# Kernel optimization log

Measured on AMD Instinct MI355X. Metric: run time of the kernel, lower is better.

## Reference

```python
import jax, jax.numpy as jnp
import numpy as np
from jax import lax

NPOINT = 1024
RADIUS = 0.2
NSAMPLE = 32


def fps(xyz, npoint):
    """Furthest point sampling on one cloud. xyz: (N,3) -> (npoint,) int32."""
    n = xyz.shape[0]
    init_d = jnp.full((n,), 1e10, xyz.dtype)

    def body(carry, _):
        dists, last_idx = carry
        last = xyz[last_idx]
        d = jnp.sum((xyz - last) ** 2, axis=-1)
        dists = jnp.minimum(dists, d)
        nxt = jnp.argmax(dists).astype(jnp.int32)
        return (dists, nxt), nxt

    (_, _), idxs = lax.scan(body, (init_d, jnp.int32(0)), None, length=npoint - 1)
    return jnp.concatenate([jnp.zeros((1,), jnp.int32), idxs])


def ball_query(xyz, new_xyz, radius, nsample):
    """First `nsample` points of xyz within `radius` of each center (pad with first hit).
    xyz: (N,3), new_xyz: (S,3) -> (S,nsample) int32."""
    n = xyz.shape[0]
    d2 = jnp.sum((new_xyz[:, None, :] - xyz[None, :, :]) ** 2, axis=-1)  # (S,N)
    cand = jnp.where(d2 < radius * radius, jnp.arange(n, dtype=jnp.int32)[None, :], n)
    idx = jnp.sort(cand, axis=1)[:, :nsample]                            # (S,K)
    first = jnp.where(idx[:, :1] == n, 0, idx[:, :1])
    return jnp.where(idx == n, first, idx)


def setup_inputs() -> dict:
    key = jax.random.key(0)
    ks = jax.random.split(key, 8)
    C_in = 64 + 3  # features + relative xyz
    W1 = jax.random.normal(ks[0], (64, C_in), jnp.float32) * (1.0 / np.sqrt(C_in))
    b1 = jnp.zeros((64,), jnp.float32)
    W2 = jax.random.normal(ks[1], (128, 64), jnp.float32) * (1.0 / np.sqrt(64))
    b2 = jnp.zeros((128,), jnp.float32)
    W3 = jax.random.normal(ks[2], (256, 128), jnp.float32) * (1.0 / np.sqrt(128))
    b3 = jnp.zeros((256,), jnp.float32)
    xyz = jax.random.uniform(ks[3], (8, 4096, 3), jnp.float32)
    features = jax.random.normal(ks[4], (8, 4096, 64), jnp.float32)
    return {"xyz": xyz, "features": features, "W1": W1, "b1": b1,
            "W2": W2, "b2": b2, "W3": W3, "b3": b3}


def reference(xyz, features, W1, b1, W2, b2, W3, b3):
    def per_batch(xyz_b, feat_b):
        fps_idx = fps(xyz_b, NPOINT)                      # (S,)
        new_xyz = xyz_b[fps_idx]                          # (S,3)
        idx = ball_query(xyz_b, new_xyz, RADIUS, NSAMPLE)  # (S,K)
        g_xyz = xyz_b[idx] - new_xyz[:, None, :]          # (S,K,3) relative coords
        g_feat = feat_b[idx]                              # (S,K,C)
        g = jnp.concatenate([g_xyz, g_feat], axis=-1)     # (S,K,3+C)
        x = jnp.transpose(g, (2, 0, 1))                   # (C',S,K)
        for W, b in ((W1, b1), (W2, b2), (W3, b3)):       # 1x1 conv + ReLU stack
            x = jax.nn.relu(jnp.einsum('oc,csk->osk', W, x) + b[:, None, None])
        return new_xyz, jnp.max(x, axis=-1), fps_idx      # max-pool over nsample

    new_xyz, new_features, sample_inds = jax.vmap(per_batch)(xyz, features)
    return new_xyz, new_features, sample_inds
```

## Files before the change

kernel.cpp:

```cpp
#include <hip/hip_runtime.h>
#include <stdint.h>

#define N_PTS 4096
#define S_PTS 1024
#define K_SAMP 32

typedef __attribute__((ext_vector_type(8))) short bf16x8;
typedef __attribute__((ext_vector_type(4))) float f32x4;

#define GT1_S 104
#define GT2_S 72
#define GT3_S 136

__device__ __forceinline__ short f2b(float f){
  unsigned u = __float_as_uint(f);
  u = u + 0x7fffu + ((u >> 16) & 1u);
  return (short)(u >> 16);
}

#define DPP_QUAD_XOR1 0xB1
#define DPP_QUAD_XOR2 0x4E
#define DPP_ROW_HMIRR 0x141
#define DPP_ROW_MIRR  0x140
#define DPP_ROW_BC15  0x142
#define DPP_ROW_BC31  0x143

template<int CTRL>
__device__ __forceinline__ unsigned long long kstep(unsigned long long k){
  unsigned lo = (unsigned)k, hi = (unsigned)(k >> 32);
  unsigned lo2 = (unsigned)__builtin_amdgcn_update_dpp((int)lo, (int)lo, CTRL, 0xF, 0xF, false);
  unsigned hi2 = (unsigned)__builtin_amdgcn_update_dpp((int)hi, (int)hi, CTRL, 0xF, 0xF, false);
  unsigned long long ok = ((unsigned long long)hi2 << 32) | lo2;
  return ok > k ? ok : k;
}

__global__ __launch_bounds__(256) void fps_kernel(const float* __restrict__ xyz,
                                                  float* __restrict__ out_newxyz,
                                                  float* __restrict__ out_inds){
  __shared__ float4 c4[N_PTS];
  __shared__ unsigned long long slots[2][4];
  const int b = blockIdx.x;
  const int t = threadIdx.x;
  const int lane = t & 63;
  const int w = t >> 6;
  const float* xb = xyz + (size_t)b * N_PTS * 3;

  float px[16], py[16], pz[16], dist[16];
#pragma unroll
  for (int j = 0; j < 16; ++j){
    int p = j * 256 + t;
    float x = xb[p*3+0], y = xb[p*3+1], z = xb[p*3+2];
    px[j] = x; py[j] = y; pz[j] = z; dist[j] = 1e10f;
    c4[p] = make_float4(x, y, z, 0.0f);
  }
  __syncthreads();

  float lx, ly, lz;
  { float4 c0 = c4[0]; lx = c0.x; ly = c0.y; lz = c0.z; }
  if (t == 0){
    out_inds[(size_t)b * S_PTS] = 0.0f;
    out_newxyz[(size_t)b*S_PTS*3 + 0] = lx;
    out_newxyz[(size_t)b*S_PTS*3 + 1] = ly;
    out_newxyz[(size_t)b*S_PTS*3 + 2] = lz;
  }

  for (int it = 1; it < S_PTS; ++it){
    float bv = -1.0f; int bj = 0;
#pragma unroll
    for (int j = 0; j < 16; ++j){
      float dx = __fsub_rn(px[j], lx);
      float dy = __fsub_rn(py[j], ly);
      float dz = __fsub_rn(pz[j], lz);
      float d  = __fadd_rn(__fadd_rn(__fmul_rn(dx,dx), __fmul_rn(dy,dy)), __fmul_rn(dz,dz));
      float nd = fminf(dist[j], d);
      dist[j] = nd;
      bool gt = nd > bv;
      bv = gt ? nd : bv;
      bj = gt ? j  : bj;
    }
    int bi = bj * 256 + t;
    unsigned long long k = ((unsigned long long)__float_as_uint(bv) << 32)
                         | (unsigned)(~bi);

    k = kstep<DPP_QUAD_XOR1>(k);
    k = kstep<DPP_QUAD_XOR2>(k);
    k = kstep<DPP_ROW_HMIRR>(k);
    k = kstep<DPP_ROW_MIRR >(k);
    k = kstep<DPP_ROW_BC15 >(k);
    k = kstep<DPP_ROW_BC31 >(k);

    if (lane == 63) slots[it & 1][w] = k;
    __syncthreads();

    unsigned long long sk = slots[it & 1][lane & 3];
    sk = kstep<DPP_QUAD_XOR1>(sk);
    sk = kstep<DPP_QUAD_XOR2>(sk);
    int cur = (int)(~(unsigned)sk);

    float4 cc = c4[cur];
    lx = cc.x; ly = cc.y; lz = cc.z;
    if (t == 0){
      out_inds[(size_t)b*S_PTS + it] = (float)cur;
      out_newxyz[((size_t)b*S_PTS + it)*3 + 0] = lx;
      out_newxyz[((size_t)b*S_PTS + it)*3 + 1] = ly;
      out_newxyz[((size_t)b*S_PTS + it)*3 + 2] = lz;
    }
  }
}

__global__ void wconv_kernel(const float* __restrict__ W1,
                             const float* __restrict__ W2,
                             const float* __restrict__ W3,
                             short* __restrict__ ws_w){
  short* w1 = ws_w;
  short* w2 = ws_w + 64*96;
  short* w3 = ws_w + 64*96 + 128*64;
  int t = blockIdx.x * blockDim.x + threadIdx.x;
  int stride = gridDim.x * blockDim.x;
  for (int i = t; i < 64*96; i += stride){
    int m = i / 96, k = i - m*96;
    float v = 0.0f;
    if (k < 64)      v = W1[m*67 + 3 + k];
    else if (k < 67) v = W1[m*67 + (k - 64)];
    w1[i] = f2b(v);
  }
  for (int i = t; i < 128*64;  i += stride) w2[i] = f2b(W2[i]);
  for (int i = t; i < 256*128; i += stride) w3[i] = f2b(W3[i]);
}

__global__ __launch_bounds__(256) void ballquery_kernel(const float* __restrict__ xyz,
                                                        const float* __restrict__ newxyz,
                                                        int* __restrict__ idx_ws){
  const int lane = threadIdx.x & 63;
  const int c = blockIdx.x * 4 + (threadIdx.x >> 6);
  const int b = c >> 10;
  const float* xb = xyz + (size_t)b * N_PTS * 3;
  const float cx = newxyz[(size_t)c*3+0];
  const float cy = newxyz[(size_t)c*3+1];
  const float cz = newxyz[(size_t)c*3+2];
  const float R2 = 0.2f * 0.2f;
  int* idxp = idx_ws + (size_t)c * K_SAMP;
  int have = 0, first = -1;
  for (int chunk = 0; chunk < 64 && have < K_SAMP; ++chunk){
    int p = chunk * 64 + lane;
    float dx = __fsub_rn(xb[p*3+0], cx);
    float dy = __fsub_rn(xb[p*3+1], cy);
    float dz = __fsub_rn(xb[p*3+2], cz);
    float d2 = __fadd_rn(__fadd_rn(__fmul_rn(dx,dx), __fmul_rn(dy,dy)), __fmul_rn(dz,dz));
    bool hit = d2 < R2;
    unsigned long long mask = __ballot(hit);
    if (mask){
      if (first < 0) first = chunk*64 + (__ffsll(mask) - 1);
      int pre = __popcll(mask & ((1ull << lane) - 1ull));
      if (hit && (have + pre) < K_SAMP) idxp[have + pre] = p;
      have += __popcll(mask);
      if (have > K_SAMP) have = K_SAMP;
    }
  }
  if (first < 0) first = 0;
  if (lane < K_SAMP - have) idxp[have + lane] = first;
}

template<int M, int KC, int KPAD, int GS_IN, int GS_OUT>
__device__ __forceinline__ void layer_mfma(const short* __restrict__ Wl,
                                           const short* gin, short* gout,
                                           const float* __restrict__ sbias_l,
                                           int w, int quad, int col){
  for (int m0 = w*16; m0 < M; m0 += 64){
    f32x4 acc0 = {0,0,0,0}, acc1 = {0,0,0,0};
#pragma unroll
    for (int kc = 0; kc < KC; ++kc){
      bf16x8 a  = *reinterpret_cast<const bf16x8*>(Wl + (size_t)(m0+col)*KPAD + kc*32 + quad*8);
      bf16x8 b0 = *reinterpret_cast<const bf16x8*>(gin + col*GS_IN + kc*32 + quad*8);
      bf16x8 b1 = *reinterpret_cast<const bf16x8*>(gin + (16+col)*GS_IN + kc*32 + quad*8);
      acc0 = __builtin_amdgcn_mfma_f32_16x16x32_bf16(a, b0, acc0, 0, 0, 0);
      acc1 = __builtin_amdgcn_mfma_f32_16x16x32_bf16(a, b1, acc1, 0, 0, 0);
    }
    int rbase = m0 + quad*4;
    unsigned long long P0 = 0ull, P1 = 0ull;
#pragma unroll
    for (int r = 0; r < 4; ++r){
      float bias = sbias_l[rbase + r];
      unsigned long long q0 = (unsigned short)f2b(fmaxf(acc0[r] + bias, 0.0f));
      unsigned long long q1 = (unsigned short)f2b(fmaxf(acc1[r] + bias, 0.0f));
      P0 |= q0 << (16*r);
      P1 |= q1 << (16*r);
    }
    *reinterpret_cast<unsigned long long*>(&gout[col*GS_OUT + rbase])      = P0;
    *reinterpret_cast<unsigned long long*>(&gout[(16+col)*GS_OUT + rbase]) = P1;
  }
}

__global__ __launch_bounds__(256) void mlp_kernel(const float* __restrict__ xyz,
                                                  const float* __restrict__ feat,
                                                  const float* __restrict__ b1,
                                                  const float* __restrict__ b2,
                                                  const float* __restrict__ b3,
                                                  const float* __restrict__ newxyz,
                                                  const int* __restrict__ idx_ws,
                                                  const short* __restrict__ ws_w,
                                                  float* __restrict__ pooled){
  __shared__ __align__(16) short gT1[32*GT1_S];
  __shared__ __align__(16) short gT2[32*GT2_S];
  __shared__ __align__(16) short gT3[32*GT3_S];
  __shared__ int   sidx[32];
  __shared__ float sbias[448];
  const int t = threadIdx.x;
  const int c = blockIdx.x;
  const int b = c >> 10;
  const int lane = t & 63;
  const int w = t >> 6;
  const int quad = lane >> 4;
  const int col = lane & 15;

  const short* w1 = ws_w;
  const short* w2 = ws_w + 64*96;
  const short* w3 = ws_w + 64*96 + 128*64;

  if (t < 32) sidx[t] = idx_ws[(size_t)c*K_SAMP + t];
  for (int i = t; i < 448; i += 256)
    sbias[i] = (i < 64) ? b1[i] : (i < 192) ? b2[i-64] : b3[i-192];
  for (int i = t; i < 32*GT1_S; i += 256) gT1[i] = 0;
  __syncthreads();

  {
    int p = t >> 3, q = t & 7;
    int src = sidx[p];
    const float* fr = feat + ((size_t)b * N_PTS + src) * 64 + q*8;
    unsigned u[4];
#pragma unroll
    for (int jj = 0; jj < 4; ++jj){
      unsigned lo = (unsigned short)f2b(fr[2*jj]);
      unsigned hi = (unsigned short)f2b(fr[2*jj+1]);
      u[jj] = lo | (hi << 16);
    }
    uint4 v; v.x = u[0]; v.y = u[1]; v.z = u[2]; v.w = u[3];
    *reinterpret_cast<uint4*>(&gT1[p*GT1_S + q*8]) = v;
  }
  if (t < 32){
    int src = sidx[t];
    const float* pr = xyz + ((size_t)b * N_PTS + src) * 3;
    float cx = newxyz[(size_t)c*3+0];
    float cy = newxyz[(size_t)c*3+1];
    float cz = newxyz[(size_t)c*3+2];
    gT1[t*GT1_S + 64] = f2b(__fsub_rn(pr[0], cx));
    gT1[t*GT1_S + 65] = f2b(__fsub_rn(pr[1], cy));
    gT1[t*GT1_S + 66] = f2b(__fsub_rn(pr[2], cz));
  }
  __syncthreads();

  layer_mfma<64, 3, 96, GT1_S, GT2_S>(w1, gT1, gT2, sbias, w, quad, col);
  __syncthreads();
  layer_mfma<128, 2, 64, GT2_S, GT3_S>(w2, gT2, gT3, sbias + 64, w, quad, col);
  __syncthreads();

  for (int m0 = w*16; m0 < 256; m0 += 64){
    f32x4 acc0 = {0,0,0,0}, acc1 = {0,0,0,0};
#pragma unroll
    for (int kc = 0; kc < 4; ++kc){
      bf16x8 a  = *reinterpret_cast<const bf16x8*>(w3 + (size_t)(m0+col)*128 + kc*32 + quad*8);
      bf16x8 b0 = *reinterpret_cast<const bf16x8*>(gT3 + col*GT3_S + kc*32 + quad*8);
      bf16x8 b1 = *reinterpret_cast<const bf16x8*>(gT3 + (16+col)*GT3_S + kc*32 + quad*8);
      acc0 = __builtin_amdgcn_mfma_f32_16x16x32_bf16(a, b0, acc0, 0, 0, 0);
      acc1 = __builtin_amdgcn_mfma_f32_16x16x32_bf16(a, b1, acc1, 0, 0, 0);
    }
    float vm[4];
#pragma unroll
    for (int r = 0; r < 4; ++r) vm[r] = fmaxf(acc0[r], acc1[r]);
#pragma unroll
    for (int off = 1; off < 16; off <<= 1){
#pragma unroll
      for (int r = 0; r < 4; ++r) vm[r] = fmaxf(vm[r], __shfl_xor(vm[r], off, 16));
    }
    if (col == 0){
#pragma unroll
      for (int r = 0; r < 4; ++r){
        int ch = m0 + quad*4 + r;
        pooled[(size_t)c*256 + ch] = fmaxf(vm[r] + sbias[192 + ch], 0.0f);
      }
    }
  }
}

__global__ __launch_bounds__(256) void transpose_kernel(const float* __restrict__ pooled,
                                                        float* __restrict__ outf){
  __shared__ float tile[64][65];
  int b  = blockIdx.z;
  int s0 = blockIdx.x * 64;
  int c0 = blockIdx.y * 64;
#pragma unroll
  for (int k = 0; k < 16; ++k){
    int idx = threadIdx.x + k*256;
    int si = idx >> 6, ci = idx & 63;
    tile[si][ci] = pooled[((size_t)b*S_PTS + s0 + si)*256 + c0 + ci];
  }
  __syncthreads();
#pragma unroll
  for (int k = 0; k < 16; ++k){
    int idx = threadIdx.x + k*256;
    int ci = idx >> 6, si = idx & 63;
    outf[((size_t)b*256 + c0 + ci)*S_PTS + s0 + si] = tile[si][ci];
  }
}

extern "C" void kernel_launch(void* const* d_in, const int* in_sizes, int n_in,
                              void* d_out, int out_size, void* d_ws, size_t ws_size,
                              hipStream_t stream){
  const float* xyz  = (const float*)d_in[0];
  const float* feat = (const float*)d_in[1];
  const float* W1   = (const float*)d_in[2];
  const float* b1   = (const float*)d_in[3];
  const float* W2   = (const float*)d_in[4];
  const float* b2   = (const float*)d_in[5];
  const float* W3   = (const float*)d_in[6];
  const float* b3   = (const float*)d_in[7];

  float* out        = (float*)d_out;
  float* out_newxyz = out;
  float* out_feat   = out + 24576;
  float* out_inds   = out + 24576 + 2097152;

  char*  ws     = (char*)d_ws;
  short* ws_w   = (short*)ws;
  int*   idx_ws = (int*)(ws + 94208);
  float* pooled = (float*)(ws + 94208 + 1048576);

  wconv_kernel<<<32, 256, 0, stream>>>(W1, W2, W3, ws_w);
  fps_kernel<<<8, 256, 0, stream>>>(xyz, out_newxyz, out_inds);
  ballquery_kernel<<<2048, 256, 0, stream>>>(xyz, out_newxyz, idx_ws);
  mlp_kernel<<<8192, 256, 0, stream>>>(xyz, feat, b1, b2, b3, out_newxyz,
                                       idx_ws, ws_w, pooled);
  transpose_kernel<<<dim3(16, 4, 8), 256, 0, stream>>>(pooled, out_feat);
}
```

Baseline: 796.8 us.

## Pack FPS distance math, tree-reduce argmax, buffer outputs in LDS

The furthest-point-sampling loop now does the distance arithmetic two points at a time with packed v_pk_add/v_pk_mul f32 instructions. The serial per-thread argmax over 16 points becomes a pairwise tree, which shortens the dependency chain. Per-iteration global stores by thread 0 are replaced by writes to an LDS ring, flushed with coalesced stores after the loop. Rounding should stay the same because packed ops are separate mul and add without FMA. Tie-breaking in the tree still favours the lower index, as the strict > did before.

```diff
diff --git a/kernel.cpp b/kernel.cpp
--- a/kernel.cpp
+++ b/kernel.cpp
@@ -7,6 +7,7 @@
 
 typedef __attribute__((ext_vector_type(8))) short bf16x8;
 typedef __attribute__((ext_vector_type(4))) float f32x4;
+typedef __attribute__((ext_vector_type(2))) float f32x2;
 
 #define GT1_S 104
 #define GT2_S 72
@@ -16,6 +17,13 @@
   unsigned u = __float_as_uint(f);
   u = u + 0x7fffu + ((u >> 16) & 1u);
   return (short)(u >> 16);
+}
+
+__device__ __forceinline__ f32x2 pk_add(f32x2 a, f32x2 b){
+  f32x2 d; asm("v_pk_add_f32 %0, %1, %2" : "=v"(d) : "v"(a), "v"(b)); return d;
+}
+__device__ __forceinline__ f32x2 pk_mul(f32x2 a, f32x2 b){
+  f32x2 d; asm("v_pk_mul_f32 %0, %1, %2" : "=v"(d) : "v"(a), "v"(b)); return d;
 }
 
 #define DPP_QUAD_XOR1 0xB1
@@ -38,6 +46,7 @@
                                                   float* __restrict__ out_newxyz,
                                                   float* __restrict__ out_inds){
   __shared__ float4 c4[N_PTS];
+  __shared__ float4 ring[S_PTS];
   __shared__ unsigned long long slots[2][4];
   const int b = blockIdx.x;
   const int t = threadIdx.x;
@@ -45,39 +54,60 @@
   const int w = t >> 6;
   const float* xb = xyz + (size_t)b * N_PTS * 3;
 
-  float px[16], py[16], pz[16], dist[16];
-#pragma unroll
-  for (int j = 0; j < 16; ++j){
-    int p = j * 256 + t;
-    float x = xb[p*3+0], y = xb[p*3+1], z = xb[p*3+2];
-    px[j] = x; py[j] = y; pz[j] = z; dist[j] = 1e10f;
-    c4[p] = make_float4(x, y, z, 0.0f);
+  f32x2 px2[8], py2[8], pz2[8], dist2[8];
+#pragma unroll
+  for (int i = 0; i < 8; ++i){
+    int p0 = (2*i)   * 256 + t;
+    int p1 = (2*i+1) * 256 + t;
+    float x0 = xb[p0*3+0], y0 = xb[p0*3+1], z0 = xb[p0*3+2];
+    float x1 = xb[p1*3+0], y1 = xb[p1*3+1], z1 = xb[p1*3+2];
+    px2[i].x = x0; px2[i].y = x1;
+    py2[i].x = y0; py2[i].y = y1;
+    pz2[i].x = z0; pz2[i].y = z1;
+    dist2[i].x = 1e10f; dist2[i].y = 1e10f;
+    c4[p0] = make_float4(x0, y0, z0, 0.0f);
+    c4[p1] = make_float4(x1, y1, z1, 0.0f);
   }
   __syncthreads();
 
   float lx, ly, lz;
   { float4 c0 = c4[0]; lx = c0.x; ly = c0.y; lz = c0.z; }
-  if (t == 0){
-    out_inds[(size_t)b * S_PTS] = 0.0f;
-    out_newxyz[(size_t)b*S_PTS*3 + 0] = lx;
-    out_newxyz[(size_t)b*S_PTS*3 + 1] = ly;
-    out_newxyz[(size_t)b*S_PTS*3 + 2] = lz;
-  }
+  if (t == 0) ring[0] = make_float4(lx, ly, lz, 0.0f);
 
   for (int it = 1; it < S_PTS; ++it){
-    float bv = -1.0f; int bj = 0;
-#pragma unroll
-    for (int j = 0; j < 16; ++j){
-      float dx = __fsub_rn(px[j], lx);
-      float dy = __fsub_rn(py[j], ly);
-      float dz = __fsub_rn(pz[j], lz);
-      float d  = __fadd_rn(__fadd_rn(__fmul_rn(dx,dx), __fmul_rn(dy,dy)), __fmul_rn(dz,dz));
-      float nd = fminf(dist[j], d);
-      dist[j] = nd;
-      bool gt = nd > bv;
-      bv = gt ? nd : bv;
-      bj = gt ? j  : bj;
-    }
+    f32x2 nlx = { -lx, -lx }, nly = { -ly, -ly }, nlz = { -lz, -lz };
+    float v8[8]; int j8[8];
+#pragma unroll
+    for (int i = 0; i < 8; ++i){
+      f32x2 dx = pk_add(px2[i], nlx);
+      f32x2 dy = pk_add(py2[i], nly);
+      f32x2 dz = pk_add(pz2[i], nlz);
+      f32x2 d2 = pk_add(pk_add(pk_mul(dx,dx), pk_mul(dy,dy)), pk_mul(dz,dz));
+      float nd0 = fminf(dist2[i].x, d2.x);
+      float nd1 = fminf(dist2[i].y, d2.y);
+      dist2[i].x = nd0; dist2[i].y = nd1;
+      bool g = nd1 > nd0;
+      v8[i] = g ? nd1 : nd0;
+      j8[i] = g ? 2*i+1 : 2*i;
+    }
+    float v4[4]; int j4[4];
+#pragma unroll
+    for (int i = 0; i < 4; ++i){
+      bool g = v8[2*i+1] > v8[2*i];
+      v4[i] = g ? v8[2*i+1] : v8[2*i];
+      j4[i] = g ? j8[2*i+1] : j8[2*i];
+    }
+    float v2a[2]; int j2a[2];
+#pragma unroll
+    for (int i = 0; i < 2; ++i){
+      bool g = v4[2*i+1] > v4[2*i];
+      v2a[i] = g ? v4[2*i+1] : v4[2*i];
+      j2a[i] = g ? j4[2*i+1] : j4[2*i];
+    }
+    bool gf = v2a[1] > v2a[0];
+    float bv = gf ? v2a[1] : v2a[0];
+    int   bj = gf ? j2a[1] : j2a[0];
+
     int bi = bj * 256 + t;
     unsigned long long k = ((unsigned long long)__float_as_uint(bv) << 32)
                          | (unsigned)(~bi);
@@ -99,12 +129,18 @@
 
     float4 cc = c4[cur];
     lx = cc.x; ly = cc.y; lz = cc.z;
-    if (t == 0){
-      out_inds[(size_t)b*S_PTS + it] = (float)cur;
-      out_newxyz[((size_t)b*S_PTS + it)*3 + 0] = lx;
-      out_newxyz[((size_t)b*S_PTS + it)*3 + 1] = ly;
-      out_newxyz[((size_t)b*S_PTS + it)*3 + 2] = lz;
-    }
+    if (t == 0) ring[it] = make_float4(lx, ly, lz, (float)cur);
+  }
+
+  __syncthreads();
+#pragma unroll
+  for (int e = 0; e < 4; ++e){
+    int i = e * 256 + t;
+    float4 v = ring[i];
+    out_inds[(size_t)b*S_PTS + i] = v.w;
+    out_newxyz[((size_t)b*S_PTS + i)*3 + 0] = v.x;
+    out_newxyz[((size_t)b*S_PTS + i)*3 + 1] = v.y;
+    out_newxyz[((size_t)b*S_PTS + i)*3 + 2] = v.z;
   }
 }
 
```

After: 1.012 ms. +27.0%, slower.

## Fuse FPS, ball query and MLP into one persistent kernel with progress flags

Applied to the files above, without the earlier changes.

Merges the FPS, ball-query and MLP kernels into a single launch. Eight blocks run FPS and publish per-batch progress counters with release stores. The remaining persistent worker blocks spin on those counters, then do ball query into shared memory followed by the MLP for each center as soon as it is available. The goal is to overlap the serial FPS with the grouping and MLP work and to remove the idx workspace round-trip, at the cost of spin-waiting and a reliance on all blocks being co-resident.

```diff
diff --git a/kernel.cpp b/kernel.cpp
--- a/kernel.cpp
+++ b/kernel.cpp
@@ -4,6 +4,7 @@
 #define N_PTS 4096
 #define S_PTS 1024
 #define K_SAMP 32
+#define NWORK 504
 
 typedef __attribute__((ext_vector_type(8))) short bf16x8;
 typedef __attribute__((ext_vector_type(4))) float f32x4;
@@ -34,84 +35,12 @@
   return ok > k ? ok : k;
 }
 
-__global__ __launch_bounds__(256) void fps_kernel(const float* __restrict__ xyz,
-                                                  float* __restrict__ out_newxyz,
-                                                  float* __restrict__ out_inds){
-  __shared__ float4 c4[N_PTS];
-  __shared__ unsigned long long slots[2][4];
-  const int b = blockIdx.x;
-  const int t = threadIdx.x;
-  const int lane = t & 63;
-  const int w = t >> 6;
-  const float* xb = xyz + (size_t)b * N_PTS * 3;
-
-  float px[16], py[16], pz[16], dist[16];
-#pragma unroll
-  for (int j = 0; j < 16; ++j){
-    int p = j * 256 + t;
-    float x = xb[p*3+0], y = xb[p*3+1], z = xb[p*3+2];
-    px[j] = x; py[j] = y; pz[j] = z; dist[j] = 1e10f;
-    c4[p] = make_float4(x, y, z, 0.0f);
-  }
-  __syncthreads();
-
-  float lx, ly, lz;
-  { float4 c0 = c4[0]; lx = c0.x; ly = c0.y; lz = c0.z; }
-  if (t == 0){
-    out_inds[(size_t)b * S_PTS] = 0.0f;
-    out_newxyz[(size_t)b*S_PTS*3 + 0] = lx;
-    out_newxyz[(size_t)b*S_PTS*3 + 1] = ly;
-    out_newxyz[(size_t)b*S_PTS*3 + 2] = lz;
-  }
-
-  for (int it = 1; it < S_PTS; ++it){
-    float bv = -1.0f; int bj = 0;
-#pragma unroll
-    for (int j = 0; j < 16; ++j){
-      float dx = __fsub_rn(px[j], lx);
-      float dy = __fsub_rn(py[j], ly);
-      float dz = __fsub_rn(pz[j], lz);
-      float d  = __fadd_rn(__fadd_rn(__fmul_rn(dx,dx), __fmul_rn(dy,dy)), __fmul_rn(dz,dz));
-      float nd = fminf(dist[j], d);
-      dist[j] = nd;
-      bool gt = nd > bv;
-      bv = gt ? nd : bv;
-      bj = gt ? j  : bj;
-    }
-    int bi = bj * 256 + t;
-    unsigned long long k = ((unsigned long long)__float_as_uint(bv) << 32)
-                         | (unsigned)(~bi);
-
-    k = kstep<DPP_QUAD_XOR1>(k);
-    k = kstep<DPP_QUAD_XOR2>(k);
-    k = kstep<DPP_ROW_HMIRR>(k);
-    k = kstep<DPP_ROW_MIRR >(k);
-    k = kstep<DPP_ROW_BC15 >(k);
-    k = kstep<DPP_ROW_BC31 >(k);
-
-    if (lane == 63) slots[it & 1][w] = k;
-    __syncthreads();
-
-    unsigned long long sk = slots[it & 1][lane & 3];
-    sk = kstep<DPP_QUAD_XOR1>(sk);
-    sk = kstep<DPP_QUAD_XOR2>(sk);
-    int cur = (int)(~(unsigned)sk);
-
-    float4 cc = c4[cur];
-    lx = cc.x; ly = cc.y; lz = cc.z;
-    if (t == 0){
-      out_inds[(size_t)b*S_PTS + it] = (float)cur;
-      out_newxyz[((size_t)b*S_PTS + it)*3 + 0] = lx;
-      out_newxyz[((size_t)b*S_PTS + it)*3 + 1] = ly;
-      out_newxyz[((size_t)b*S_PTS + it)*3 + 2] = lz;
-    }
-  }
-}
-
 __global__ void wconv_kernel(const float* __restrict__ W1,
                              const float* __restrict__ W2,
                              const float* __restrict__ W3,
-                             short* __restrict__ ws_w){
+                             short* __restrict__ ws_w,
+                             int* __restrict__ progress){
+  if (blockIdx.x == 0 && threadIdx.x < 8) progress[threadIdx.x] = 0;
   short* w1 = ws_w;
   short* w2 = ws_w + 64*96;
   short* w3 = ws_w + 64*96 + 128*64;
@@ -128,39 +57,6 @@
   for (int i = t; i < 256*128; i += stride) w3[i] = f2b(W3[i]);
 }
 
-__global__ __launch_bounds__(256) void ballquery_kernel(const float* __restrict__ xyz,
-                                                        const float* __restrict__ newxyz,
-                                                        int* __restrict__ idx_ws){
-  const int lane = threadIdx.x & 63;
-  const int c = blockIdx.x * 4 + (threadIdx.x >> 6);
-  const int b = c >> 10;
-  const float* xb = xyz + (size_t)b * N_PTS * 3;
-  const float cx = newxyz[(size_t)c*3+0];
-  const float cy = newxyz[(size_t)c*3+1];
-  const float cz = newxyz[(size_t)c*3+2];
-  const float R2 = 0.2f * 0.2f;
-  int* idxp = idx_ws + (size_t)c * K_SAMP;
-  int have = 0, first = -1;
-  for (int chunk = 0; chunk < 64 && have < K_SAMP; ++chunk){
-    int p = chunk * 64 + lane;
-    float dx = __fsub_rn(xb[p*3+0], cx);
-    float dy = __fsub_rn(xb[p*3+1], cy);
-    float dz = __fsub_rn(xb[p*3+2], cz);
-    float d2 = __fadd_rn(__fadd_rn(__fmul_rn(dx,dx), __fmul_rn(dy,dy)), __fmul_rn(dz,dz));
-    bool hit = d2 < R2;
-    unsigned long long mask = __ballot(hit);
-    if (mask){
-      if (first < 0) first = chunk*64 + (__ffsll(mask) - 1);
-      int pre = __popcll(mask & ((1ull << lane) - 1ull));
-      if (hit && (have + pre) < K_SAMP) idxp[have + pre] = p;
-      have += __popcll(mask);
-      if (have > K_SAMP) have = K_SAMP;
-    }
-  }
-  if (first < 0) first = 0;
-  if (lane < K_SAMP - have) idxp[have + lane] = first;
-}
-
 template<int M, int KC, int KPAD, int GS_IN, int GS_OUT>
 __device__ __forceinline__ void layer_mfma(const short* __restrict__ Wl,
                                            const short* gin, short* gout,
@@ -191,92 +87,198 @@
   }
 }
 
-__global__ __launch_bounds__(256) void mlp_kernel(const float* __restrict__ xyz,
-                                                  const float* __restrict__ feat,
-                                                  const float* __restrict__ b1,
-                                                  const float* __restrict__ b2,
-                                                  const float* __restrict__ b3,
-                                                  const float* __restrict__ newxyz,
-                                                  const int* __restrict__ idx_ws,
-                                                  const short* __restrict__ ws_w,
-                                                  float* __restrict__ pooled){
-  __shared__ __align__(16) short gT1[32*GT1_S];
-  __shared__ __align__(16) short gT2[32*GT2_S];
-  __shared__ __align__(16) short gT3[32*GT3_S];
-  __shared__ int   sidx[32];
-  __shared__ float sbias[448];
+__global__ __launch_bounds__(256) void fused_kernel(
+    const float* __restrict__ xyz, const float* __restrict__ feat,
+    const float* __restrict__ b1, const float* __restrict__ b2,
+    const float* __restrict__ b3, const short* __restrict__ ws_w,
+    float* __restrict__ out_newxyz, float* __restrict__ out_inds,
+    int* __restrict__ progress, float* __restrict__ pooled){
+
+  __shared__ __align__(16) union ShU {
+    struct { float4 c4[N_PTS]; unsigned long long slots[2][4]; } f;
+    struct { short gT1[32*GT1_S]; short gT2[32*GT2_S]; short gT3[32*GT3_S];
+             int sidx[K_SAMP]; float sbias[448]; } m;
+  } sh;
+
   const int t = threadIdx.x;
-  const int c = blockIdx.x;
-  const int b = c >> 10;
   const int lane = t & 63;
   const int w = t >> 6;
+
+  if (blockIdx.x < 8){
+    const int b = blockIdx.x;
+    const float* xb = xyz + (size_t)b * N_PTS * 3;
+
+    float px[16], py[16], pz[16], dist[16];
+#pragma unroll
+    for (int j = 0; j < 16; ++j){
+      int p = j * 256 + t;
+      float x = xb[p*3+0], y = xb[p*3+1], z = xb[p*3+2];
+      px[j] = x; py[j] = y; pz[j] = z; dist[j] = 1e10f;
+      sh.f.c4[p] = make_float4(x, y, z, 0.0f);
+    }
+    __syncthreads();
+
+    float lx, ly, lz;
+    { float4 c0 = sh.f.c4[0]; lx = c0.x; ly = c0.y; lz = c0.z; }
+    if (t == 0){
+      out_inds[(size_t)b * S_PTS] = 0.0f;
+      out_newxyz[(size_t)b*S_PTS*3 + 0] = lx;
+      out_newxyz[(size_t)b*S_PTS*3 + 1] = ly;
+      out_newxyz[(size_t)b*S_PTS*3 + 2] = lz;
+      __hip_atomic_store(&progress[b], 1, __ATOMIC_RELEASE, __HIP_MEMORY_SCOPE_AGENT);
+    }
+
+    for (int it = 1; it < S_PTS; ++it){
+      float bv = -1.0f; int bj = 0;
+#pragma unroll
+      for (int j = 0; j < 16; ++j){
+        float dx = __fsub_rn(px[j], lx);
+        float dy = __fsub_rn(py[j], ly);
+        float dz = __fsub_rn(pz[j], lz);
+        float d  = __fadd_rn(__fadd_rn(__fmul_rn(dx,dx), __fmul_rn(dy,dy)), __fmul_rn(dz,dz));
+        float nd = fminf(dist[j], d);
+        dist[j] = nd;
+        bool gt = nd > bv;
+        bv = gt ? nd : bv;
+        bj = gt ? j  : bj;
+      }
+      int bi = bj * 256 + t;
+      unsigned long long k = ((unsigned long long)__float_as_uint(bv) << 32)
+                           | (unsigned)(~bi);
+
+      k = kstep<DPP_QUAD_XOR1>(k);
+      k = kstep<DPP_QUAD_XOR2>(k);
+      k = kstep<DPP_ROW_HMIRR>(k);
+      k = kstep<DPP_ROW_MIRR >(k);
+      k = kstep<DPP_ROW_BC15 >(k);
+      k = kstep<DPP_ROW_BC31 >(k);
+
+      if (lane == 63) sh.f.slots[it & 1][w] = k;
+      __syncthreads();
+
+      unsigned long long sk = sh.f.slots[it & 1][lane & 3];
+      sk = kstep<DPP_QUAD_XOR1>(sk);
+      sk = kstep<DPP_QUAD_XOR2>(sk);
+      int cur = (int)(~(unsigned)sk);
+
+      float4 cc = sh.f.c4[cur];
+      lx = cc.x; ly = cc.y; lz = cc.z;
+      if (t == 0){
+        out_inds[(size_t)b*S_PTS + it] = (float)cur;
+        out_newxyz[((size_t)b*S_PTS + it)*3 + 0] = lx;
+        out_newxyz[((size_t)b*S_PTS + it)*3 + 1] = ly;
+        out_newxyz[((size_t)b*S_PTS + it)*3 + 2] = lz;
+        __hip_atomic_store(&progress[b], it + 1, __ATOMIC_RELEASE, __HIP_MEMORY_SCOPE_AGENT);
+      }
+    }
+    return;
+  }
+
+  const int wid = blockIdx.x - 8;
   const int quad = lane >> 4;
   const int col = lane & 15;
-
   const short* w1 = ws_w;
   const short* w2 = ws_w + 64*96;
   const short* w3 = ws_w + 64*96 + 128*64;
 
-  if (t < 32) sidx[t] = idx_ws[(size_t)c*K_SAMP + t];
   for (int i = t; i < 448; i += 256)
-    sbias[i] = (i < 64) ? b1[i] : (i < 192) ? b2[i-64] : b3[i-192];
-  for (int i = t; i < 32*GT1_S; i += 256) gT1[i] = 0;
-  __syncthreads();
-
-  {
-    int p = t >> 3, q = t & 7;
-    int src = sidx[p];
-    const float* fr = feat + ((size_t)b * N_PTS + src) * 64 + q*8;
-    unsigned u[4];
-#pragma unroll
-    for (int jj = 0; jj < 4; ++jj){
-      unsigned lo = (unsigned short)f2b(fr[2*jj]);
-      unsigned hi = (unsigned short)f2b(fr[2*jj+1]);
-      u[jj] = lo | (hi << 16);
-    }
-    uint4 v; v.x = u[0]; v.y = u[1]; v.z = u[2]; v.w = u[3];
-    *reinterpret_cast<uint4*>(&gT1[p*GT1_S + q*8]) = v;
-  }
-  if (t < 32){
-    int src = sidx[t];
-    const float* pr = xyz + ((size_t)b * N_PTS + src) * 3;
-    float cx = newxyz[(size_t)c*3+0];
-    float cy = newxyz[(size_t)c*3+1];
-    float cz = newxyz[(size_t)c*3+2];
-    gT1[t*GT1_S + 64] = f2b(__fsub_rn(pr[0], cx));
-    gT1[t*GT1_S + 65] = f2b(__fsub_rn(pr[1], cy));
-    gT1[t*GT1_S + 66] = f2b(__fsub_rn(pr[2], cz));
-  }
-  __syncthreads();
-
-  layer_mfma<64, 3, 96, GT1_S, GT2_S>(w1, gT1, gT2, sbias, w, quad, col);
-  __syncthreads();
-  layer_mfma<128, 2, 64, GT2_S, GT3_S>(w2, gT2, gT3, sbias + 64, w, quad, col);
-  __syncthreads();
-
-  for (int m0 = w*16; m0 < 256; m0 += 64){
-    f32x4 acc0 = {0,0,0,0}, acc1 = {0,0,0,0};
-#pragma unroll
-    for (int kc = 0; kc < 4; ++kc){
-      bf16x8 a  = *reinterpret_cast<const bf16x8*>(w3 + (size_t)(m0+col)*128 + kc*32 + quad*8);
-      bf16x8 b0 = *reinterpret_cast<const bf16x8*>(gT3 + col*GT3_S + kc*32 + quad*8);
-      bf16x8 b1 = *reinterpret_cast<const bf16x8*>(gT3 + (16+col)*GT3_S + kc*32 + quad*8);
-      acc0 = __builtin_amdgcn_mfma_f32_16x16x32_bf16(a, b0, acc0, 0, 0, 0);
-      acc1 = __builtin_amdgcn_mfma_f32_16x16x32_bf16(a, b1, acc1, 0, 0, 0);
-    }
-    float vm[4];
-#pragma unroll
-    for (int r = 0; r < 4; ++r) vm[r] = fmaxf(acc0[r], acc1[r]);
-#pragma unroll
-    for (int off = 1; off < 16; off <<= 1){
-#pragma unroll
-      for (int r = 0; r < 4; ++r) vm[r] = fmaxf(vm[r], __shfl_xor(vm[r], off, 16));
-    }
-    if (col == 0){
-#pragma unroll
-      for (int r = 0; r < 4; ++r){
-        int ch = m0 + quad*4 + r;
-        pooled[(size_t)c*256 + ch] = fmaxf(vm[r] + sbias[192 + ch], 0.0f);
+    sh.m.sbias[i] = (i < 64) ? b1[i] : (i < 192) ? b2[i-64] : b3[i-192];
+  for (int i = t; i < 32*GT1_S; i += 256) sh.m.gT1[i] = 0;
+
+  for (int c = wid; c < 8*S_PTS; c += NWORK){
+    const int b = c >> 10;
+    const int s = c & (S_PTS - 1);
+
+    if (t == 0){
+      while (__hip_atomic_load(&progress[b], __ATOMIC_RELAXED, __HIP_MEMORY_SCOPE_AGENT) <= s)
+        __builtin_amdgcn_s_sleep(2);
+    }
+    __syncthreads();
+    __builtin_amdgcn_fence(__ATOMIC_ACQUIRE, "agent");
+
+    if (w == 0){
+      const float* xb = xyz + (size_t)b * N_PTS * 3;
+      const float cx = out_newxyz[(size_t)c*3+0];
+      const float cy = out_newxyz[(size_t)c*3+1];
+      const float cz = out_newxyz[(size_t)c*3+2];
+      const float R2 = 0.2f * 0.2f;
+      int have = 0, first = -1;
+      for (int chunk = 0; chunk < 64 && have < K_SAMP; ++chunk){
+        int p = chunk * 64 + lane;
+        float dx = __fsub_rn(xb[p*3+0], cx);
+        float dy = __fsub_rn(xb[p*3+1], cy);
+        float dz = __fsub_rn(xb[p*3+2], cz);
+        float d2 = __fadd_rn(__fadd_rn(__fmul_rn(dx,dx), __fmul_rn(dy,dy)), __fmul_rn(dz,dz));
+        bool hit = d2 < R2;
+        unsigned long long mask = __ballot(hit);
+        if (mask){
+          if (first < 0) first = chunk*64 + (__ffsll(mask) - 1);
+          int pre = __popcll(mask & ((1ull << lane) - 1ull));
+          if (hit && (have + pre) < K_SAMP) sh.m.sidx[have + pre] = p;
+          have += __popcll(mask);
+          if (have > K_SAMP) have = K_SAMP;
+        }
+      }
+      if (first < 0) first = 0;
+      if (lane < K_SAMP - have) sh.m.sidx[have + lane] = first;
+    }
+    __syncthreads();
+
+    {
+      int p = t >> 3, q = t & 7;
+      int src = sh.m.sidx[p];
+      const float* fr = feat + ((size_t)b * N_PTS + src) * 64 + q*8;
+      unsigned u[4];
+#pragma unroll
+      for (int jj = 0; jj < 4; ++jj){
+        unsigned lo = (unsigned short)f2b(fr[2*jj]);
+        unsigned hi = (unsigned short)f2b(fr[2*jj+1]);
+        u[jj] = lo | (hi << 16);
+      }
+      uint4 v; v.x = u[0]; v.y = u[1]; v.z = u[2]; v.w = u[3];
+      *reinterpret_cast<uint4*>(&sh.m.gT1[p*GT1_S + q*8]) = v;
+    }
+    if (t < 32){
+      int src = sh.m.sidx[t];
+      const float* pr = xyz + ((size_t)b * N_PTS + src) * 3;
+      float cx = out_newxyz[(size_t)c*3+0];
+      float cy = out_newxyz[(size_t)c*3+1];
+      float cz = out_newxyz[(size_t)c*3+2];
+      sh.m.gT1[t*GT1_S + 64] = f2b(__fsub_rn(pr[0], cx));
+      sh.m.gT1[t*GT1_S + 65] = f2b(__fsub_rn(pr[1], cy));
+      sh.m.gT1[t*GT1_S + 66] = f2b(__fsub_rn(pr[2], cz));
+    }
+    __syncthreads();
+
+    layer_mfma<64, 3, 96, GT1_S, GT2_S>(w1, sh.m.gT1, sh.m.gT2, sh.m.sbias, w, quad, col);
+    __syncthreads();
+    layer_mfma<128, 2, 64, GT2_S, GT3_S>(w2, sh.m.gT2, sh.m.gT3, sh.m.sbias + 64, w, quad, col);
+    __syncthreads();
+
+    for (int m0 = w*16; m0 < 256; m0 += 64){
+      f32x4 acc0 = {0,0,0,0}, acc1 = {0,0,0,0};
+#pragma unroll
+      for (int kc = 0; kc < 4; ++kc){
+        bf16x8 a  = *reinterpret_cast<const bf16x8*>(w3 + (size_t)(m0+col)*128 + kc*32 + quad*8);
+        bf16x8 b0 = *reinterpret_cast<const bf16x8*>(sh.m.gT3 + col*GT3_S + kc*32 + quad*8);
+        bf16x8 b1 = *reinterpret_cast<const bf16x8*>(sh.m.gT3 + (16+col)*GT3_S + kc*32 + quad*8);
+        acc0 = __builtin_amdgcn_mfma_f32_16x16x32_bf16(a, b0, acc0, 0, 0, 0);
+        acc1 = __builtin_amdgcn_mfma_f32_16x16x32_bf16(a, b1, acc1, 0, 0, 0);
+      }
+      float vm[4];
+#pragma unroll
+      for (int r = 0; r < 4; ++r) vm[r] = fmaxf(acc0[r], acc1[r]);
+#pragma unroll
+      for (int off = 1; off < 16; off <<= 1){
+#pragma unroll
+        for (int r = 0; r < 4; ++r) vm[r] = fmaxf(vm[r], __shfl_xor(vm[r], off, 16));
+      }
+      if (col == 0){
+#pragma unroll
+        for (int r = 0; r < 4; ++r){
+          int ch = m0 + quad*4 + r;
+          pooled[(size_t)c*256 + ch] = fmaxf(vm[r] + sh.m.sbias[192 + ch], 0.0f);
+        }
       }
     }
   }
@@ -320,15 +322,13 @@
   float* out_feat   = out + 24576;
   float* out_inds   = out + 24576 + 2097152;
 
-  char*  ws     = (char*)d_ws;
-  short* ws_w   = (short*)ws;
-  int*   idx_ws = (int*)(ws + 94208);
-  float* pooled = (float*)(ws + 94208 + 1048576);
-
-  wconv_kernel<<<32, 256, 0, stream>>>(W1, W2, W3, ws_w);
-  fps_kernel<<<8, 256, 0, stream>>>(xyz, out_newxyz, out_inds);
-  ballquery_kernel<<<2048, 256, 0, stream>>>(xyz, out_newxyz, idx_ws);
-  mlp_kernel<<<8192, 256, 0, stream>>>(xyz, feat, b1, b2, b3, out_newxyz,
-                                       idx_ws, ws_w, pooled);
+  char*  ws       = (char*)d_ws;
+  short* ws_w     = (short*)ws;
+  int*   progress = (int*)(ws + 94208);
+  float* pooled   = (float*)(ws + 94208 + 1048576);
+
+  wconv_kernel<<<32, 256, 0, stream>>>(W1, W2, W3, ws_w, progress);
+  fused_kernel<<<8 + NWORK, 256, 0, stream>>>(xyz, feat, b1, b2, b3, ws_w,
+                                              out_newxyz, out_inds, progress, pooled);
   transpose_kernel<<<dim3(16, 4, 8), 256, 0, stream>>>(pooled, out_feat);
 }
```

Result: slower. 1.636 ms (+105.4%).
